# Optimization experiments

Hardware: AMD Instinct MI355X
Metric: run time of the kernel (lower is better)

## Reference

```python
import jax, jax.numpy as jnp
import numpy as np

COEF = 0.1   # cfg.MODEL.SS.COEF
P, U, V, F = 8, 256, 256, 256 * 49  # pairs, u-proposals, v-proposals, ROI feat dim (256*7*7)


def setup_inputs() -> dict:
    key = jax.random.key(0)
    k1, k2 = jax.random.split(key)
    feat_u = jax.random.normal(k1, (P, U, F), dtype=jnp.float32)
    feat_v = jax.random.normal(k2, (P, V, F), dtype=jnp.float32)
    return {"feat_u": feat_u, "feat_v": feat_v}


def reference(feat_u, feat_v):
    # Pairwise squared L2 distance without materializing the O(U*V*F) expanded tensor:
    # ||u - v||^2 = ||u||^2 + ||v||^2 - 2 u.v
    uu = jnp.sum(feat_u * feat_u, axis=-1)                 # [P, U]
    vv = jnp.sum(feat_v * feat_v, axis=-1)                 # [P, V]
    uv = jnp.einsum('puf,pvf->puv', feat_u, feat_v)        # [P, U, V]
    dist = (uu[:, :, None] + vv[:, None, :] - 2.0 * uv) * COEF
    # Original applies softmax directly to the (positive) distances along v.
    score = jax.nn.softmax(dist, axis=-1)                  # [P, U, V]
    # neg_fea = score @ feat_v  (soft-kNN aggregation)
    neg_fea = jnp.einsum('puv,pvf->puf', score, feat_v)    # [P, U, F]
    pos_fea = feat_u.reshape(-1, F)                        # [P*U, F]
    # forward returns torch.cat([pos_fea, neg_fea], 0)
    return jnp.concatenate([pos_fea, neg_fea.reshape(-1, F)], axis=0)
```

## Files before the change

### kernel.cpp

```cpp
#include <hip/hip_runtime.h>
#include <cstdint>
#include <cstddef>

#define P_DIM 8
#define U_DIM 256
#define V_DIM 256
#define F_DIM 12544

typedef __attribute__((ext_vector_type(8))) short short8;
typedef __attribute__((ext_vector_type(8))) _Float16 half8;
typedef __attribute__((ext_vector_type(4))) float f32x4;

#define MFMA16B(a, b, c) __builtin_amdgcn_mfma_f32_16x16x32_bf16((a), (b), (c), 0, 0, 0)
#define MFMA16H(a, b, c) __builtin_amdgcn_mfma_f32_16x16x32_f16((a), (b), (c), 0, 0, 0)

#define GLOAD16(gsrc, ldsbase)                                                \
  __builtin_amdgcn_global_load_lds(                                           \
      (const __attribute__((address_space(1))) void*)(gsrc),                  \
      (__attribute__((address_space(3))) void*)(ldsbase), 16, 0, 0)

__device__ __forceinline__ unsigned short f2bf(float x) {
  unsigned u = __builtin_bit_cast(unsigned, x);
  u += 0x7FFFu + ((u >> 16) & 1u);
  return (unsigned short)(u >> 16);
}
__device__ __forceinline__ unsigned short f2h(float x) {
  return __builtin_bit_cast(unsigned short, (_Float16)x);
}

__global__ __launch_bounds__(256) void prep_fv(const float* __restrict__ fv,
                                               unsigned short* __restrict__ fvT,
                                               unsigned short* __restrict__ fvH,
                                               float* __restrict__ vvpart) {
  __shared__ unsigned short tile[64][65];
  __shared__ float vvp[64];
  int f0 = blockIdx.x * 64, v0 = blockIdx.y * 64, p = blockIdx.z;
  const float* src = fv + (size_t)p * V_DIM * F_DIM;
  unsigned short* dstH = fvH + (size_t)p * V_DIM * F_DIM;
  int t = threadIdx.x;
  #pragma unroll
  for (int i = 0; i < 4; ++i) {
    int g = t + i * 256;
    int r = g >> 4;
    int c4 = (g & 15) * 4;
    float4 x = *(const float4*)(src + (size_t)(v0 + r) * F_DIM + f0 + c4);
    tile[r][c4 + 0] = f2bf(x.x);
    tile[r][c4 + 1] = f2bf(x.y);
    tile[r][c4 + 2] = f2bf(x.z);
    tile[r][c4 + 3] = f2bf(x.w);
    ushort4 h;
    h.x = f2h(x.x); h.y = f2h(x.y); h.z = f2h(x.z); h.w = f2h(x.w);
    *(ushort4*)(dstH + (size_t)(v0 + r) * F_DIM + f0 + c4) = h;
    float ps = x.x * x.x + x.y * x.y + x.z * x.z + x.w * x.w;
    ps += __shfl_xor(ps, 1); ps += __shfl_xor(ps, 2);
    ps += __shfl_xor(ps, 4); ps += __shfl_xor(ps, 8);
    if ((t & 15) == 0) vvp[r] = ps;
  }
  __syncthreads();
  if (t < 64)
    vvpart[((size_t)blockIdx.x * P_DIM + p) * V_DIM + v0 + t] = vvp[t];
  unsigned short* dst = fvT + (size_t)p * F_DIM * V_DIM;
  #pragma unroll
  for (int i = 0; i < 2; ++i) {
    int g = t + i * 256;
    int f = g >> 3;
    int v8 = (g & 7) * 8;
    short8 o;
    #pragma unroll
    for (int j = 0; j < 8; ++j) o[j] = (short)tile[v8 + j][f];
    *(short8*)(dst + (size_t)(f0 + f) * V_DIM + v0 + v8) = o;
  }
}

__global__ __launch_bounds__(256) void vv_reduce(const float* __restrict__ vvpart,
                                                 float* __restrict__ vv) {
  int p = blockIdx.x >> 2;
  int vb = (blockIdx.x & 3) * 64;
  int vl = threadIdx.x & 63;
  int v = vb + vl;
  int js = threadIdx.x >> 6;
  float s = 0.f;
  for (int j = js; j < F_DIM / 64; j += 4)
    s += vvpart[((size_t)j * P_DIM + p) * V_DIM + v];
  __shared__ float red[4][64];
  red[js][vl] = s;
  __syncthreads();
  if (threadIdx.x < 64)
    vv[p * V_DIM + v] = red[0][vl] + red[1][vl] + red[2][vl] + red[3][vl];
}

__global__ __launch_bounds__(256) void copy_fu(const float4* __restrict__ src,
                                               float4* __restrict__ dst,
                                               ushort4* __restrict__ fuH, int n4) {
  for (int i = blockIdx.x * 256 + threadIdx.x; i < n4; i += gridDim.x * 256) {
    float4 x = src[i];
    dst[i] = x;
    ushort4 h;
    h.x = f2h(x.x); h.y = f2h(x.y); h.z = f2h(x.z); h.w = f2h(x.w);
    fuH[i] = h;
  }
}

__global__ __launch_bounds__(256, 2) void uv_gemm(const unsigned short* __restrict__ fuH,
                                                  const unsigned short* __restrict__ fvH,
                                                  float* __restrict__ part,
                                                  int splitk, int chunk) {
  int nwg = gridDim.x;
  int q = nwg >> 3, r = nwg & 7;
  int xcd = blockIdx.x & 7, ofs = blockIdx.x >> 3;
  int wgid = (xcd < r ? xcd * (q + 1) : r * (q + 1) + (xcd - r) * q) + ofs;
  int nt = wgid & 1, mt = (wgid >> 1) & 1, p = (wgid >> 2) & 7, ks = wgid >> 5;

  const unsigned short* A = fuH + ((size_t)p * U_DIM + mt * 128) * F_DIM;
  const unsigned short* B = fvH + ((size_t)p * V_DIM + nt * 128) * F_DIM;
  int k0 = ks * chunk;
  int nkt = chunk >> 6;

  __shared__ short AS[2][128 * 64], BS[2][128 * 64];

  int tid = threadIdx.x, lane = tid & 63, wid = tid >> 6;
  int wm = wid >> 1, wn = wid & 1;
  int rl = lane & 15;
  f32x4 acc[4][4] = {};

#define STAGE(Abuf, Bbuf, kg)                                                 \
  do {                                                                        \
    _Pragma("unroll") for (int j = 0; j < 4; ++j) {                           \
      int g = tid + j * 256;                                                  \
      int row = g >> 3;                                                       \
      int sc = (g & 7) ^ (row & 7);                                           \
      int ldsbase = (wid * 64 + j * 256) * 16;                                \
      GLOAD16(A + (size_t)row * F_DIM + (kg) + sc * 8, (char*)(Abuf) + ldsbase);\
      GLOAD16(B + (size_t)row * F_DIM + (kg) + sc * 8, (char*)(Bbuf) + ldsbase);\
    }                                                                         \
  } while (0)

  STAGE(AS[0], BS[0], k0);
  __syncthreads();
  int cur = 0;
  for (int kt = 0; kt < nkt; ++kt) {
    if (kt + 1 < nkt)
      STAGE(AS[cur ^ 1], BS[cur ^ 1], k0 + (kt + 1) * 64);
    const char* Ap = (const char*)AS[cur];
    const char* Bp = (const char*)BS[cur];
    #pragma unroll
    for (int kk = 0; kk < 2; ++kk) {
      int kbyte = kk * 64 + (lane >> 4) * 16;
      half8 ah[4], bh[4];
      #pragma unroll
      for (int m = 0; m < 4; ++m) {
        int row = wm * 64 + m * 16 + rl;
        int off = (row * 128 + kbyte) ^ ((row & 7) << 4);
        ah[m] = *(const half8*)(Ap + off);
      }
      #pragma unroll
      for (int n = 0; n < 4; ++n) {
        int row = wn * 64 + n * 16 + rl;
        int off = (row * 128 + kbyte) ^ ((row & 7) << 4);
        bh[n] = *(const half8*)(Bp + off);
      }
      #pragma unroll
      for (int m = 0; m < 4; ++m)
        #pragma unroll
        for (int n = 0; n < 4; ++n)
          acc[m][n] = MFMA16H(ah[m], bh[n], acc[m][n]);
    }
    __syncthreads();
    cur ^= 1;
  }
#undef STAGE
  float* dst = part + ((size_t)ks * P_DIM + p) * U_DIM * V_DIM;
  int rq = lane >> 4;
  #pragma unroll
  for (int m = 0; m < 4; ++m)
    #pragma unroll
    for (int n = 0; n < 4; ++n)
      #pragma unroll
      for (int i = 0; i < 4; ++i) {
        int u = mt * 128 + wm * 64 + m * 16 + rq * 4 + i;
        int v = nt * 128 + wn * 64 + n * 16 + rl;
        dst[(size_t)u * V_DIM + v] = acc[m][n][i];
      }
}

__global__ __launch_bounds__(256) void reduce_softmax(const float* __restrict__ part,
                                                      const float* __restrict__ vv,
                                                      unsigned short* __restrict__ score,
                                                      int splitk) {
  int u = blockIdx.x & 255, p = blockIdx.x >> 8;
  int v = threadIdx.x;
  size_t base = ((size_t)p * U_DIM + u) * V_DIM + v;
  float s = 0.f;
  for (int k = 0; k < splitk; ++k)
    s += part[(size_t)k * (P_DIM * U_DIM * V_DIM) + base];
  float logit = 0.1f * vv[p * V_DIM + v] - 0.2f * s;
  float m = logit;
  #pragma unroll
  for (int off = 32; off >= 1; off >>= 1) m = fmaxf(m, __shfl_xor(m, off));
  __shared__ float red[4], red2[4];
  int lane = v & 63, wid = v >> 6;
  if (lane == 0) red[wid] = m;
  __syncthreads();
  m = fmaxf(fmaxf(red[0], red[1]), fmaxf(red[2], red[3]));
  float e = __expf(logit - m);
  float tsum = e;
  #pragma unroll
  for (int off = 32; off >= 1; off >>= 1) tsum += __shfl_xor(tsum, off);
  if (lane == 0) red2[wid] = tsum;
  __syncthreads();
  tsum = red2[0] + red2[1] + red2[2] + red2[3];
  score[base] = f2bf(e / tsum);
}

__global__ __launch_bounds__(256, 2) void pv_gemm(const unsigned short* __restrict__ score,
                                                  const unsigned short* __restrict__ fvT,
                                                  float* __restrict__ outneg) {
  int my = blockIdx.x;
  int bx = blockIdx.y;
  int p = blockIdx.z;
  int n0 = bx * 64;
  const unsigned short* Sc = score + ((size_t)p * U_DIM + my * 128) * V_DIM;
  const unsigned short* Bt = fvT + ((size_t)p * F_DIM + n0) * V_DIM;
  __shared__ short Bs[64 * 256];
  char* Bsp = (char*)Bs;
  int tid = threadIdx.x, lane = tid & 63, wid = tid >> 6;
  int rl = lane & 15, rq = lane >> 4;

  #pragma unroll
  for (int j = 0; j < 8; ++j) {
    int g = tid + j * 256;
    int row = g >> 5;
    int c = g & 31;
    int sc = c ^ (row & 7);
    int ldsbase = (wid * 64 + j * 256) * 16;
    GLOAD16(Bt + (size_t)row * V_DIM + sc * 8, Bsp + ldsbase);
  }

  short8 a[2][8];
  #pragma unroll
  for (int m = 0; m < 2; ++m)
    #pragma unroll
    for (int k = 0; k < 8; ++k)
      a[m][k] = *(const short8*)(Sc + (size_t)(wid * 32 + m * 16 + rl) * V_DIM
                                 + k * 32 + rq * 8);
  __syncthreads();

  f32x4 acc[2][4] = {};
  #pragma unroll
  for (int k = 0; k < 8; ++k) {
    #pragma unroll
    for (int n = 0; n < 4; ++n) {
      int row = n * 16 + rl;
      short8 b = *(const short8*)(Bsp + row * 512
                                  + ((k * 64 + rq * 16) ^ ((row & 7) << 4)));
      acc[0][n] = MFMA16B(a[0][k], b, acc[0][n]);
      acc[1][n] = MFMA16B(a[1][k], b, acc[1][n]);
    }
  }

  float* dst = outneg + ((size_t)p * U_DIM + my * 128) * F_DIM;
  #pragma unroll
  for (int m = 0; m < 2; ++m)
    #pragma unroll
    for (int n = 0; n < 4; ++n)
      #pragma unroll
      for (int i = 0; i < 4; ++i) {
        int u = wid * 32 + m * 16 + rq * 4 + i;
        int f = n0 + n * 16 + rl;
        dst[(size_t)u * F_DIM + f] = acc[m][n][i];
      }
}

extern "C" void kernel_launch(void* const* d_in, const int* in_sizes, int n_in,
                              void* d_out, int out_size, void* d_ws, size_t ws_size,
                              hipStream_t stream) {
  const float* fu = (const float*)d_in[0];
  const float* fv = (const float*)d_in[1];
  float* out = (float*)d_out;
  char* ws = (char*)d_ws;

  const size_t HVF = (size_t)P_DIM * F_DIM * V_DIM * 2;
  float* vv = (float*)ws;
  unsigned short* score = (unsigned short*)(ws + 8192);
  unsigned short* fvT = (unsigned short*)(ws + 8192 + 1048576);
  unsigned short* fuH = (unsigned short*)(ws + 8192 + 1048576 + HVF);
  unsigned short* fvH = (unsigned short*)(ws + 8192 + 1048576 + 2 * HVF);
  size_t vvpartBase = 8192 + 1048576 + 3 * HVF;
  float* vvpart = (float*)(ws + vvpartBase);
  size_t partBase = vvpartBase + (size_t)(F_DIM / 64) * P_DIM * V_DIM * 4;
  float* part = (float*)(ws + partBase);

  const size_t puv4 = (size_t)P_DIM * U_DIM * V_DIM * 4;
  int splitk = 1;
  const int cands[6] = {28, 14, 7, 4, 2, 1};
  for (int i = 0; i < 6; ++i) {
    if (partBase + (size_t)cands[i] * puv4 <= ws_size) { splitk = cands[i]; break; }
  }
  int chunk = F_DIM / splitk;

  prep_fv<<<dim3(F_DIM / 64, V_DIM / 64, P_DIM), 256, 0, stream>>>(fv, fvT, fvH,
                                                                   vvpart);
  vv_reduce<<<P_DIM * 4, 256, 0, stream>>>(vvpart, vv);
  int n4 = (P_DIM * U_DIM * F_DIM) / 4;
  copy_fu<<<2048, 256, 0, stream>>>((const float4*)fu, (float4*)out,
                                    (ushort4*)fuH, n4);
  uv_gemm<<<splitk * 32, 256, 0, stream>>>(fuH, fvH, part, splitk, chunk);
  reduce_softmax<<<P_DIM * U_DIM, 256, 0, stream>>>(part, vv, score, splitk);
  pv_gemm<<<dim3(2, F_DIM / 64, P_DIM), 256, 0, stream>>>(
      score, fvT, out + (size_t)P_DIM * U_DIM * F_DIM);
}
```

Measured before the change: 210.5 us.

## Stage uv_gemm tiles through registers instead of direct global-to-LDS loads; cap splitk at 14

Replaces the global_load_lds async copies in the uv GEMM with ordinary vector global loads into registers. Those registers are written into swizzled LDS after the MFMA compute of the current tile, so the next tile's load latency overlaps the math. It also removes splitk=28 from the candidate list, which halves the grid and the partial-sum traffic into reduce_softmax while lengthening each block's K loop. The trade-off is higher register pressure and fewer workgroups, which may lower occupancy or leave CUs idle.

```diff
diff --git a/kernel.cpp b/kernel.cpp
--- a/kernel.cpp
+++ b/kernel.cpp
@@ -122,25 +122,36 @@
   int wm = wid >> 1, wn = wid & 1;
   int rl = lane & 15;
   f32x4 acc[4][4] = {};
-
-#define STAGE(Abuf, Bbuf, kg)                                                 \
+  short8 ra[4], rb[4];
+
+#define LOADR(kg)                                                             \
   do {                                                                        \
     _Pragma("unroll") for (int j = 0; j < 4; ++j) {                           \
       int g = tid + j * 256;                                                  \
-      int row = g >> 3;                                                       \
-      int sc = (g & 7) ^ (row & 7);                                           \
-      int ldsbase = (wid * 64 + j * 256) * 16;                                \
-      GLOAD16(A + (size_t)row * F_DIM + (kg) + sc * 8, (char*)(Abuf) + ldsbase);\
-      GLOAD16(B + (size_t)row * F_DIM + (kg) + sc * 8, (char*)(Bbuf) + ldsbase);\
+      int row = g >> 3, c = g & 7;                                            \
+      ra[j] = *(const short8*)(A + (size_t)row * F_DIM + (kg) + c * 8);       \
+      rb[j] = *(const short8*)(B + (size_t)row * F_DIM + (kg) + c * 8);       \
     }                                                                         \
   } while (0)
 
-  STAGE(AS[0], BS[0], k0);
+#define WRITES(buf)                                                           \
+  do {                                                                        \
+    _Pragma("unroll") for (int j = 0; j < 4; ++j) {                           \
+      int g = tid + j * 256;                                                  \
+      int row = g >> 3, c = g & 7;                                            \
+      int off = (row * 128 + c * 16) ^ ((row & 7) << 4);                      \
+      *(short8*)((char*)AS[buf] + off) = ra[j];                               \
+      *(short8*)((char*)BS[buf] + off) = rb[j];                               \
+    }                                                                         \
+  } while (0)
+
+  LOADR(k0);
+  WRITES(0);
   __syncthreads();
   int cur = 0;
   for (int kt = 0; kt < nkt; ++kt) {
-    if (kt + 1 < nkt)
-      STAGE(AS[cur ^ 1], BS[cur ^ 1], k0 + (kt + 1) * 64);
+    bool more = (kt + 1 < nkt);
+    if (more) LOADR(k0 + (kt + 1) * 64);
     const char* Ap = (const char*)AS[cur];
     const char* Bp = (const char*)BS[cur];
     #pragma unroll
@@ -165,10 +176,12 @@
         for (int n = 0; n < 4; ++n)
           acc[m][n] = MFMA16H(ah[m], bh[n], acc[m][n]);
     }
+    if (more) WRITES(cur ^ 1);
     __syncthreads();
     cur ^= 1;
   }
-#undef STAGE
+#undef LOADR
+#undef WRITES
   float* dst = part + ((size_t)ks * P_DIM + p) * U_DIM * V_DIM;
   int rq = lane >> 4;
   #pragma unroll
@@ -292,8 +305,8 @@
 
   const size_t puv4 = (size_t)P_DIM * U_DIM * V_DIM * 4;
   int splitk = 1;
-  const int cands[6] = {28, 14, 7, 4, 2, 1};
-  for (int i = 0; i < 6; ++i) {
+  const int cands[5] = {14, 7, 4, 2, 1};
+  for (int i = 0; i < 5; ++i) {
     if (partBase + (size_t)cands[i] * puv4 <= ws_size) { splitk = cands[i]; break; }
   }
   int chunk = F_DIM / splitk;
```

Result: faster. 196.2 us (-6.8%).

## Load uv_gemm MFMA operands directly from global into registers, drop LDS staging

Applied to the files above, without the earlier changes.

Replaces the LDS double-buffered staging in uv_gemm with direct per-lane global loads into registers, ping-ponged across two register sets so the next k-tile loads while the current one feeds the MFMAs. This removes the LDS traffic and the __syncthreads barriers. The cost is that A and B tiles are no longer shared through LDS, so each wave fetches its own operands from global/L2 and register pressure rises. Split-K is also capped at 14, which halves the grid and the partial-sum traffic but lowers parallelism.

```diff
diff --git a/kernel.cpp b/kernel.cpp
--- a/kernel.cpp
+++ b/kernel.cpp
@@ -116,61 +116,55 @@
   int k0 = ks * chunk;
   int nkt = chunk >> 6;
 
-  __shared__ short AS[2][128 * 64], BS[2][128 * 64];
-
   int tid = threadIdx.x, lane = tid & 63, wid = tid >> 6;
   int wm = wid >> 1, wn = wid & 1;
-  int rl = lane & 15;
+  int rl = lane & 15, rq = lane >> 4;
+
+  const unsigned short* Ar[4];
+  const unsigned short* Br[4];
+  #pragma unroll
+  for (int m = 0; m < 4; ++m)
+    Ar[m] = A + (size_t)(wm * 64 + m * 16 + rl) * F_DIM + rq * 8;
+  #pragma unroll
+  for (int n = 0; n < 4; ++n)
+    Br[n] = B + (size_t)(wn * 64 + n * 16 + rl) * F_DIM + rq * 8;
+
   f32x4 acc[4][4] = {};
-
-#define STAGE(Abuf, Bbuf, kg)                                                 \
+  short8 a0[4][2], b0[4][2], a1[4][2], b1[4][2];
+
+#define LOADF(sa, sb, kg)                                                     \
   do {                                                                        \
-    _Pragma("unroll") for (int j = 0; j < 4; ++j) {                           \
-      int g = tid + j * 256;                                                  \
-      int row = g >> 3;                                                       \
-      int sc = (g & 7) ^ (row & 7);                                           \
-      int ldsbase = (wid * 64 + j * 256) * 16;                                \
-      GLOAD16(A + (size_t)row * F_DIM + (kg) + sc * 8, (char*)(Abuf) + ldsbase);\
-      GLOAD16(B + (size_t)row * F_DIM + (kg) + sc * 8, (char*)(Bbuf) + ldsbase);\
-    }                                                                         \
+    _Pragma("unroll") for (int m = 0; m < 4; ++m)                             \
+      _Pragma("unroll") for (int kk = 0; kk < 2; ++kk)                        \
+        sa[m][kk] = *(const short8*)(Ar[m] + (kg) + kk * 32);                 \
+    _Pragma("unroll") for (int n = 0; n < 4; ++n)                             \
+      _Pragma("unroll") for (int kk = 0; kk < 2; ++kk)                        \
+        sb[n][kk] = *(const short8*)(Br[n] + (kg) + kk * 32);                 \
   } while (0)
 
-  STAGE(AS[0], BS[0], k0);
-  __syncthreads();
-  int cur = 0;
-  for (int kt = 0; kt < nkt; ++kt) {
-    if (kt + 1 < nkt)
-      STAGE(AS[cur ^ 1], BS[cur ^ 1], k0 + (kt + 1) * 64);
-    const char* Ap = (const char*)AS[cur];
-    const char* Bp = (const char*)BS[cur];
-    #pragma unroll
-    for (int kk = 0; kk < 2; ++kk) {
-      int kbyte = kk * 64 + (lane >> 4) * 16;
-      half8 ah[4], bh[4];
-      #pragma unroll
-      for (int m = 0; m < 4; ++m) {
-        int row = wm * 64 + m * 16 + rl;
-        int off = (row * 128 + kbyte) ^ ((row & 7) << 4);
-        ah[m] = *(const half8*)(Ap + off);
-      }
-      #pragma unroll
-      for (int n = 0; n < 4; ++n) {
-        int row = wn * 64 + n * 16 + rl;
-        int off = (row * 128 + kbyte) ^ ((row & 7) << 4);
-        bh[n] = *(const half8*)(Bp + off);
-      }
-      #pragma unroll
-      for (int m = 0; m < 4; ++m)
-        #pragma unroll
-        for (int n = 0; n < 4; ++n)
-          acc[m][n] = MFMA16H(ah[m], bh[n], acc[m][n]);
+#define MFMA_TILE(sa, sb)                                                     \
+  do {                                                                        \
+    _Pragma("unroll") for (int kk = 0; kk < 2; ++kk)                          \
+      _Pragma("unroll") for (int m = 0; m < 4; ++m)                           \
+        _Pragma("unroll") for (int n = 0; n < 4; ++n)                         \
+          acc[m][n] = MFMA16H(__builtin_bit_cast(half8, sa[m][kk]),           \
+                              __builtin_bit_cast(half8, sb[n][kk]),           \
+                              acc[m][n]);                                     \
+  } while (0)
+
+  LOADF(a0, b0, k0);
+  for (int kt = 0; kt < nkt; kt += 2) {
+    if (kt + 1 < nkt) LOADF(a1, b1, k0 + (kt + 1) * 64);
+    MFMA_TILE(a0, b0);
+    if (kt + 1 < nkt) {
+      if (kt + 2 < nkt) LOADF(a0, b0, k0 + (kt + 2) * 64);
+      MFMA_TILE(a1, b1);
     }
-    __syncthreads();
-    cur ^= 1;
-  }
-#undef STAGE
+  }
+#undef LOADF
+#undef MFMA_TILE
+
   float* dst = part + ((size_t)ks * P_DIM + p) * U_DIM * V_DIM;
-  int rq = lane >> 4;
   #pragma unroll
   for (int m = 0; m < 4; ++m)
     #pragma unroll
@@ -292,8 +286,8 @@
 
   const size_t puv4 = (size_t)P_DIM * U_DIM * V_DIM * 4;
   int splitk = 1;
-  const int cands[6] = {28, 14, 7, 4, 2, 1};
-  for (int i = 0; i < 6; ++i) {
+  const int cands[5] = {14, 7, 4, 2, 1};
+  for (int i = 0; i < 5; ++i) {
     if (partBase + (size_t)cands[i] * puv4 <= ws_size) { splitk = cands[i]; break; }
   }
   int chunk = F_DIM / splitk;
```

Measured after the change: 222.8 us. 1.06x slower.
